# Performance work log

Measured on AMD Instinct MI355X. Metric: run time of the kernel, lower is better.

Reference implementation:

```python
import jax, jax.numpy as jnp
import numpy as np

HEAD = 8  # number of attention heads (init kwarg)


def setup_inputs() -> dict:
    key = jax.random.key(0)
    k1, k2, k3 = jax.random.split(key, 3)
    b, H, W, c = 8, 32, 32, 512
    dim = 512
    x = jax.random.normal(k1, (b, H, W, c), dtype=jnp.float32)
    # 1x1 Conv == per-pixel matmul over channels
    w_qkv = jax.random.normal(k2, (c, 3 * dim), dtype=jnp.float32) * (c ** -0.5)
    w_out = jax.random.normal(k3, (dim, dim), dtype=jnp.float32) * (dim ** -0.5)
    b_out = jnp.zeros((dim,), dtype=jnp.float32)
    return {"x": x, "w_qkv": w_qkv, "w_out": w_out, "b_out": b_out}


def reference(x, w_qkv, w_out, b_out):
    b, H, W, c = x.shape
    n = H * W
    # QKV 1x1-conv projection (no bias)
    qkv = jnp.einsum('bhwc,cd->bhwd', x, w_qkv)          # (b, H, W, 3*dim)
    qkv = qkv.reshape(b, n, HEAD, -1)                     # (b, n, head, 3*dh)
    q, k, v = jnp.split(qkv, 3, axis=-1)                  # each (b, n, head, dh)
    scale = b ** -0.5  # NOTE: source scales by batch size, reproduced faithfully
    attn = jax.nn.softmax(jnp.einsum('bihd,bjhd->bhij', q, k) * scale, axis=-1)
    out = jnp.einsum('bhij,bjhd->bihd', attn, v)          # (b, n, head, dh)
    out = out.reshape(b, H, W, -1)                        # (b, H, W, dim)
    # output 1x1-conv projection (with bias)
    return jnp.einsum('bhwc,cd->bhwd', out, w_out) + b_out
```

## Files before the change

### kernel.cpp

```cpp
#include <hip/hip_runtime.h>
#include <hip/hip_bf16.h>

typedef __bf16 bf16x8_t __attribute__((ext_vector_type(8)));
typedef float  f32x4_t  __attribute__((ext_vector_type(4)));
typedef short  s16x4_t  __attribute__((ext_vector_type(4)));
typedef short  s16x8_t  __attribute__((ext_vector_type(8)));

#define NTOK   1024
#define CDIM   512
#define QKVDIM 1536
#define NHEAD  8
#define DHEAD  64
#define C1EXP  0.51007088f
#define C2EXP  34.624681f

__device__ __forceinline__ float b2f(short s) {
    unsigned int u = ((unsigned int)(unsigned short)s) << 16;
    float f; __builtin_memcpy(&f, &u, 4); return f;
}
__device__ __forceinline__ short f2b(float f) {
    __bf16 h = (__bf16)f; short s; __builtin_memcpy(&s, &h, 2); return s;
}

__global__ __launch_bounds__(256) void cvt_w(
    const float* __restrict__ wq, const float* __restrict__ wo,
    short* __restrict__ wqbT, short* __restrict__ wobT)
{
    const int b = blockIdx.x;
    const int t = threadIdx.x;
    const int kk = t & 63, grp = t >> 6;
    if (b < 192) {
        const int K0 = (b & 7) * 64, N0 = (b >> 3) * 64;
#pragma unroll
        for (int s = 0; s < 16; ++s) {
            int n = N0 + grp * 16 + s;
            wqbT[(size_t)n * 512 + K0 + kk] = f2b(wq[(size_t)(K0 + kk) * 1536 + n]);
        }
    } else {
        const int b2 = b - 192;
        const int K0 = (b2 & 7) * 64, N0 = (b2 >> 3) * 64;
#pragma unroll
        for (int s = 0; s < 16; ++s) {
            int n = N0 + grp * 16 + s;
            wobT[(size_t)n * 512 + K0 + kk] = f2b(wo[(size_t)(K0 + kk) * 512 + n]);
        }
    }
}

__global__ __launch_bounds__(256) void gemm_qkv(
    const float* __restrict__ X, const short* __restrict__ Bt,
    short* __restrict__ qk, short* __restrict__ vT)
{
    __shared__ __align__(16) short Al[128 * 64];
    __shared__ __align__(16) short Bl[128 * 64];

    const int t = threadIdx.x;
    const int bid = blockIdx.x;
    const int xcd = bid & 7, jpos = bid >> 3;
    const int tm = xcd * 8 + jpos / 12;
    const int tn = jpos % 12;
    const int N0 = tn * 128, M0 = tm * 128;
    const int w = t >> 6, lane = t & 63;
    const int quad = lane >> 4, mr = lane & 15;
    const int wm = (w >> 1) * 64, wn = (w & 1) * 64;

    int srow[4], soff[4];
#pragma unroll
    for (int r = 0; r < 4; ++r) {
        int ci = r * 256 + t;
        srow[r] = ci >> 3;
        soff[r] = (ci & 7) * 8;
    }
    const float* Ag = X  + (size_t)M0 * 512;
    const short* Bg = Bt + (size_t)N0 * 512;

    float4  fa[4][2];
    s16x8_t br[4];
#pragma unroll
    for (int r = 0; r < 4; ++r) {
        const float* pa = Ag + (size_t)srow[r] * 512 + soff[r];
        fa[r][0] = *(const float4*)pa;
        fa[r][1] = *(const float4*)(pa + 4);
        br[r] = *(const s16x8_t*)(Bg + (size_t)srow[r] * 512 + soff[r]);
    }

    f32x4_t acc[4][4];
#pragma unroll
    for (int ms = 0; ms < 4; ++ms)
#pragma unroll
        for (int ns = 0; ns < 4; ++ns) acc[ms][ns] = f32x4_t{0.f,0.f,0.f,0.f};

#pragma unroll 1
    for (int kc = 0; kc < 8; ++kc) {
        __syncthreads();
#pragma unroll
        for (int r = 0; r < 4; ++r) {
            int lds = srow[r] * 64 + (((soff[r] >> 3) ^ (srow[r] & 7)) * 8);
            s16x8_t va;
            va[0] = f2b(fa[r][0].x); va[1] = f2b(fa[r][0].y);
            va[2] = f2b(fa[r][0].z); va[3] = f2b(fa[r][0].w);
            va[4] = f2b(fa[r][1].x); va[5] = f2b(fa[r][1].y);
            va[6] = f2b(fa[r][1].z); va[7] = f2b(fa[r][1].w);
            *(s16x8_t*)(Al + lds) = va;
            *(s16x8_t*)(Bl + lds) = br[r];
        }
        __syncthreads();
        if (kc < 7) {
            int k0 = (kc + 1) * 64;
#pragma unroll
            for (int r = 0; r < 4; ++r) {
                const float* pa = Ag + (size_t)srow[r] * 512 + k0 + soff[r];
                fa[r][0] = *(const float4*)pa;
                fa[r][1] = *(const float4*)(pa + 4);
                br[r] = *(const s16x8_t*)(Bg + (size_t)srow[r] * 512 + k0 + soff[r]);
            }
        }
#pragma unroll
        for (int kh = 0; kh < 2; ++kh) {
            bf16x8_t af[4], bf[4];
#pragma unroll
            for (int ms = 0; ms < 4; ++ms) {
                int rr = wm + ms * 16 + mr;
                af[ms] = *(const bf16x8_t*)(Al + rr * 64 + (((kh * 4 + quad) ^ (rr & 7)) * 8));
            }
#pragma unroll
            for (int ns = 0; ns < 4; ++ns) {
                int rr = wn + ns * 16 + mr;
                bf[ns] = *(const bf16x8_t*)(Bl + rr * 64 + (((kh * 4 + quad) ^ (rr & 7)) * 8));
            }
#pragma unroll
            for (int ms = 0; ms < 4; ++ms)
#pragma unroll
                for (int ns = 0; ns < 4; ++ns)
                    acc[ms][ns] = __builtin_amdgcn_mfma_f32_16x16x32_bf16(
                        af[ms], bf[ns], acc[ms][ns], 0, 0, 0);
        }
    }

#pragma unroll
    for (int ms = 0; ms < 4; ++ms) {
        int row = M0 + wm + ms * 16 + quad * 4;
        int bb = row >> 10, ti = row & 1023;
#pragma unroll
        for (int ns = 0; ns < 4; ++ns) {
            int c0 = N0 + wn + ns * 16;
            int hh = c0 / 192, r0 = c0 % 192;
            if (r0 < 128) {
                size_t base = (size_t)row * 1024 + hh * 128 + r0 + mr;
#pragma unroll
                for (int i = 0; i < 4; ++i)
                    qk[base + (size_t)i * 1024] = f2b(acc[ms][ns][i]);
            } else {
                s16x4_t v4;
#pragma unroll
                for (int i = 0; i < 4; ++i) v4[i] = f2b(acc[ms][ns][i]);
                *(s16x4_t*)(vT + ((size_t)(bb * 8 + hh) * 64 + (r0 - 128) + mr) * 1024 + ti) = v4;
            }
        }
    }
}

template <int N, bool BIAS, bool OUTF32>
__global__ __launch_bounds__(256) void gemm128(
    const short* __restrict__ A, const short* __restrict__ Bt,
    const float* __restrict__ bias, void* __restrict__ C)
{
    __shared__ __align__(16) short Al[128 * 64];
    __shared__ __align__(16) short Bl[128 * 64];

    constexpr int TNT = N / 128;
    const int t = threadIdx.x;
    const int bid = blockIdx.x;
    const int xcd = bid & 7, jpos = bid >> 3;
    const int tm = xcd * 8 + jpos / TNT;
    const int tn = jpos % TNT;
    const int N0 = tn * 128, M0 = tm * 128;
    const int w = t >> 6, lane = t & 63;
    const int quad = lane >> 4, mr = lane & 15;
    const int wm = (w >> 1) * 64, wn = (w & 1) * 64;

    int srow[4], soff[4];
#pragma unroll
    for (int r = 0; r < 4; ++r) {
        int ci = r * 256 + t;
        srow[r] = ci >> 3;
        soff[r] = (ci & 7) * 8;
    }
    const short* Ag = A  + (size_t)M0 * 512;
    const short* Bg = Bt + (size_t)N0 * 512;

    s16x8_t ar[4], br[4];
#pragma unroll
    for (int r = 0; r < 4; ++r) {
        ar[r] = *(const s16x8_t*)(Ag + (size_t)srow[r] * 512 + soff[r]);
        br[r] = *(const s16x8_t*)(Bg + (size_t)srow[r] * 512 + soff[r]);
    }

    f32x4_t acc[4][4];
#pragma unroll
    for (int ms = 0; ms < 4; ++ms)
#pragma unroll
        for (int ns = 0; ns < 4; ++ns) acc[ms][ns] = f32x4_t{0.f,0.f,0.f,0.f};

#pragma unroll 1
    for (int kc = 0; kc < 8; ++kc) {
        __syncthreads();
#pragma unroll
        for (int r = 0; r < 4; ++r) {
            int lds = srow[r] * 64 + (((soff[r] >> 3) ^ (srow[r] & 7)) * 8);
            *(s16x8_t*)(Al + lds) = ar[r];
            *(s16x8_t*)(Bl + lds) = br[r];
        }
        __syncthreads();
        if (kc < 7) {
            int k0 = (kc + 1) * 64;
#pragma unroll
            for (int r = 0; r < 4; ++r) {
                ar[r] = *(const s16x8_t*)(Ag + (size_t)srow[r] * 512 + k0 + soff[r]);
                br[r] = *(const s16x8_t*)(Bg + (size_t)srow[r] * 512 + k0 + soff[r]);
            }
        }
#pragma unroll
        for (int kh = 0; kh < 2; ++kh) {
            bf16x8_t af[4], bf[4];
#pragma unroll
            for (int ms = 0; ms < 4; ++ms) {
                int rr = wm + ms * 16 + mr;
                af[ms] = *(const bf16x8_t*)(Al + rr * 64 + (((kh * 4 + quad) ^ (rr & 7)) * 8));
            }
#pragma unroll
            for (int ns = 0; ns < 4; ++ns) {
                int rr = wn + ns * 16 + mr;
                bf[ns] = *(const bf16x8_t*)(Bl + rr * 64 + (((kh * 4 + quad) ^ (rr & 7)) * 8));
            }
#pragma unroll
            for (int ms = 0; ms < 4; ++ms)
#pragma unroll
                for (int ns = 0; ns < 4; ++ns)
                    acc[ms][ns] = __builtin_amdgcn_mfma_f32_16x16x32_bf16(
                        af[ms], bf[ns], acc[ms][ns], 0, 0, 0);
        }
    }

#pragma unroll
    for (int ms = 0; ms < 4; ++ms) {
        int row = M0 + wm + ms * 16 + quad * 4;
#pragma unroll
        for (int ns = 0; ns < 4; ++ns) {
            int col = N0 + wn + ns * 16 + mr;
            float bz = BIAS ? bias[col] : 0.f;
#pragma unroll
            for (int i = 0; i < 4; ++i) {
                if constexpr (OUTF32)
                    ((float*)C)[(size_t)(row + i) * N + col] = acc[ms][ns][i] + bz;
                else
                    ((short*)C)[(size_t)(row + i) * N + col] = f2b(acc[ms][ns][i]);
            }
        }
    }
}

__global__ __launch_bounds__(256) void attn_st(
    const short* __restrict__ qk, const short* __restrict__ vT,
    short* __restrict__ aout)
{
    __shared__ __align__(16) short Kl[64 * 72];
    __shared__ __align__(16) short Vt[64 * 72];
    __shared__ __align__(16) short Pl[4][16 * 72];

    const int t = threadIdx.x;
    const int g = blockIdx.x;
    const int qt = (g >> 3) & 15;
    const int bh = ((g >> 7) << 3) | (g & 7);
    const int h = bh & 7, b = bh >> 3;
    const int w = t >> 6, lane = t & 63;
    const int quad = lane >> 4, mr = lane & 15;

    const size_t qbase = (size_t)(b * NTOK + qt * 64 + w * 16 + mr) * 1024 + h * 128;
    const bf16x8_t qf0 = *(const bf16x8_t*)(qk + qbase + quad * 8);
    const bf16x8_t qf1 = *(const bf16x8_t*)(qk + qbase + 32 + quad * 8);

    s16x8_t ones_s;
#pragma unroll
    for (int e = 0; e < 8; ++e) ones_s[e] = 0x3F80;
    const bf16x8_t onesv = *(const bf16x8_t*)&ones_s;

    f32x4_t L4 = f32x4_t{0.f, 0.f, 0.f, 0.f};
    f32x4_t O[4];
#pragma unroll
    for (int d = 0; d < 4; ++d) O[d] = f32x4_t{0.f, 0.f, 0.f, 0.f};

    short* Pm = Pl[w];

    const int r0i = t >> 3, r1i = r0i + 32, c8 = (t & 7) * 8;
    const size_t kgbase = (size_t)(b * NTOK) * 1024 + h * 128 + 64 + c8;
    const size_t vgbase = (size_t)(b * 8 + h) * 64 * 1024 + c8;

    s16x8_t k0r, k1r, v0r, v1r;
    k0r = *(const s16x8_t*)(qk + kgbase + (size_t)r0i * 1024);
    k1r = *(const s16x8_t*)(qk + kgbase + (size_t)r1i * 1024);
    v0r = *(const s16x8_t*)(vT + vgbase + (size_t)r0i * 1024);
    v1r = *(const s16x8_t*)(vT + vgbase + (size_t)r1i * 1024);

#pragma unroll 1
    for (int jt = 0; jt < 16; ++jt) {
        *(s16x8_t*)(Kl + r0i * 72 + c8) = k0r;
        *(s16x8_t*)(Kl + r1i * 72 + c8) = k1r;
        *(s16x8_t*)(Vt + r0i * 72 + c8) = v0r;
        *(s16x8_t*)(Vt + r1i * 72 + c8) = v1r;
        __syncthreads();

        if (jt < 15) {
            int j0n = (jt + 1) * 64;
            k0r = *(const s16x8_t*)(qk + kgbase + (size_t)(j0n + r0i) * 1024);
            k1r = *(const s16x8_t*)(qk + kgbase + (size_t)(j0n + r1i) * 1024);
            v0r = *(const s16x8_t*)(vT + vgbase + (size_t)r0i * 1024 + j0n);
            v1r = *(const s16x8_t*)(vT + vgbase + (size_t)r1i * 1024 + j0n);
        }

        f32x4_t s[4];
        __builtin_amdgcn_s_setprio(1);
#pragma unroll
        for (int jj = 0; jj < 4; ++jj) {
            const short* kb = Kl + (jj * 16 + mr) * 72 + quad * 8;
            f32x4_t a0 = __builtin_amdgcn_mfma_f32_16x16x32_bf16(
                *(const bf16x8_t*)kb, qf0, f32x4_t{0.f,0.f,0.f,0.f}, 0, 0, 0);
            s[jj] = __builtin_amdgcn_mfma_f32_16x16x32_bf16(
                *(const bf16x8_t*)(kb + 32), qf1, a0, 0, 0, 0);
        }
        __builtin_amdgcn_s_setprio(0);

#pragma unroll
        for (int jj = 0; jj < 4; ++jj) {
            s16x4_t pv;
#pragma unroll
            for (int r = 0; r < 4; ++r)
                pv[r] = f2b(__builtin_amdgcn_exp2f(s[jj][r] * C1EXP - C2EXP));
            *(s16x4_t*)(Pm + mr * 72 + jj * 16 + quad * 4) = pv;
        }

        bf16x8_t pa0 = *(const bf16x8_t*)(Pm + mr * 72 + quad * 8);
        bf16x8_t pa1 = *(const bf16x8_t*)(Pm + mr * 72 + 32 + quad * 8);

        __builtin_amdgcn_s_setprio(1);
        L4 = __builtin_amdgcn_mfma_f32_16x16x32_bf16(pa0, onesv, L4, 0, 0, 0);
        L4 = __builtin_amdgcn_mfma_f32_16x16x32_bf16(pa1, onesv, L4, 0, 0, 0);
#pragma unroll
        for (int dt = 0; dt < 4; ++dt) {
            const short* vb = Vt + (dt * 16 + mr) * 72 + quad * 8;
            O[dt] = __builtin_amdgcn_mfma_f32_16x16x32_bf16(
                pa0, *(const bf16x8_t*)vb, O[dt], 0, 0, 0);
            O[dt] = __builtin_amdgcn_mfma_f32_16x16x32_bf16(
                pa1, *(const bf16x8_t*)(vb + 32), O[dt], 0, 0, 0);
        }
        __builtin_amdgcn_s_setprio(0);
        __syncthreads();
    }

#pragma unroll
    for (int dt = 0; dt < 4; ++dt)
#pragma unroll
        for (int i = 0; i < 4; ++i)
            Pm[(quad * 4 + i) * 72 + dt * 16 + mr] = f2b(O[dt][i] * (1.f / L4[i]));
    __syncthreads();

    const int q2 = lane >> 2, h2 = lane & 3;
    const size_t tok = (size_t)(b * NTOK + qt * 64 + w * 16 + q2);
    s16x8_t o0 = *(const s16x8_t*)(Pm + q2 * 72 + h2 * 16);
    s16x8_t o1 = *(const s16x8_t*)(Pm + q2 * 72 + h2 * 16 + 8);
    *(s16x8_t*)(aout + tok * CDIM + h * DHEAD + h2 * 16)     = o0;
    *(s16x8_t*)(aout + tok * CDIM + h * DHEAD + h2 * 16 + 8) = o1;
}

extern "C" void kernel_launch(void* const* d_in, const int* in_sizes, int n_in,
                              void* d_out, int out_size, void* d_ws, size_t ws_size,
                              hipStream_t stream)
{
    const float* x     = (const float*)d_in[0];
    const float* w_qkv = (const float*)d_in[1];
    const float* w_out = (const float*)d_in[2];
    const float* b_out = (const float*)d_in[3];
    for (int i = 0; i < n_in; ++i) {
        if      (in_sizes[i] == 4194304) x     = (const float*)d_in[i];
        else if (in_sizes[i] ==  786432) w_qkv = (const float*)d_in[i];
        else if (in_sizes[i] ==  262144) w_out = (const float*)d_in[i];
        else if (in_sizes[i] ==     512) b_out = (const float*)d_in[i];
    }

    short* qk   = (short*)d_ws;
    short* vT   = (short*)((char*)d_ws + (size_t)8192 * 1024 * 2);
    short* aout = (short*)((char*)d_ws + (size_t)8192 * 1024 * 2 + (size_t)64 * 64 * 1024 * 2);
    short* wobT = (short*)((char*)d_ws + (size_t)33 * 1024 * 1024 + (size_t)1664 * 1024);
    short* wqbT = (short*)d_out + (size_t)8192 * 512;

    cvt_w<<<256, 256, 0, stream>>>(w_qkv, w_out, wqbT, wobT);

    gemm_qkv<<<768, 256, 0, stream>>>(x, wqbT, qk, vT);

    attn_st<<<1024, 256, 0, stream>>>(qk, vT, aout);

    gemm128<CDIM, true, true>
        <<<(CDIM / 128) * 64, 256, 0, stream>>>(aout, wobT, b_out, d_out);
}
```

Baseline: 135.7 us.

## Enlarge attention tiles to 128 queries and 128 keys per block

The attention kernel now runs 512-thread blocks (8 waves) that each handle 128 query rows and stage 128-key K/V tiles per iteration, which halves the grid and the number of loop iterations and barriers. Each K/V tile loaded into shared memory is reused by twice as many query rows, cutting global K/V traffic per query. The QK^T, exp and P writeback are interleaved per 16-key sub-tile. In exchange, shared memory per block and register pressure rise, and there are fewer blocks to spread across CUs, which can reduce occupancy and latency hiding.

```diff
diff --git a/kernel.cpp b/kernel.cpp
--- a/kernel.cpp
+++ b/kernel.cpp
@@ -260,23 +260,23 @@
     }
 }
 
-__global__ __launch_bounds__(256) void attn_st(
+__global__ __launch_bounds__(512, 4) void attn_st(
     const short* __restrict__ qk, const short* __restrict__ vT,
     short* __restrict__ aout)
 {
-    __shared__ __align__(16) short Kl[64 * 72];
-    __shared__ __align__(16) short Vt[64 * 72];
-    __shared__ __align__(16) short Pl[4][16 * 72];
+    __shared__ __align__(16) short Kl[128 * 72];
+    __shared__ __align__(16) short Vt[64 * 136];
+    __shared__ __align__(16) short Pl[8][16 * 136];
 
     const int t = threadIdx.x;
     const int g = blockIdx.x;
-    const int qt = (g >> 3) & 15;
-    const int bh = ((g >> 7) << 3) | (g & 7);
+    const int qt = (g >> 3) & 7;
+    const int bh = ((g >> 6) << 3) | (g & 7);
     const int h = bh & 7, b = bh >> 3;
     const int w = t >> 6, lane = t & 63;
     const int quad = lane >> 4, mr = lane & 15;
 
-    const size_t qbase = (size_t)(b * NTOK + qt * 64 + w * 16 + mr) * 1024 + h * 128;
+    const size_t qbase = (size_t)(b * NTOK + qt * 128 + w * 16 + mr) * 1024 + h * 128;
     const bf16x8_t qf0 = *(const bf16x8_t*)(qk + qbase + quad * 8);
     const bf16x8_t qf1 = *(const bf16x8_t*)(qk + qbase + 32 + quad * 8);
 
@@ -292,68 +292,70 @@
 
     short* Pm = Pl[w];
 
-    const int r0i = t >> 3, r1i = r0i + 32, c8 = (t & 7) * 8;
-    const size_t kgbase = (size_t)(b * NTOK) * 1024 + h * 128 + 64 + c8;
-    const size_t vgbase = (size_t)(b * 8 + h) * 64 * 1024 + c8;
+    const int kr0 = t >> 3, kr1 = kr0 + 64;
+    const int kc8 = (t & 7) * 8;
+    const int vr0 = t >> 4, vr1 = vr0 + 32;
+    const int vc8 = (t & 15) * 8;
+
+    const size_t kg = (size_t)(b * NTOK) * 1024 + h * 128 + 64 + kc8;
+    const size_t vg = (size_t)(b * 8 + h) * 64 * 1024 + vc8;
 
     s16x8_t k0r, k1r, v0r, v1r;
-    k0r = *(const s16x8_t*)(qk + kgbase + (size_t)r0i * 1024);
-    k1r = *(const s16x8_t*)(qk + kgbase + (size_t)r1i * 1024);
-    v0r = *(const s16x8_t*)(vT + vgbase + (size_t)r0i * 1024);
-    v1r = *(const s16x8_t*)(vT + vgbase + (size_t)r1i * 1024);
+    k0r = *(const s16x8_t*)(qk + kg + (size_t)kr0 * 1024);
+    k1r = *(const s16x8_t*)(qk + kg + (size_t)kr1 * 1024);
+    v0r = *(const s16x8_t*)(vT + vg + (size_t)vr0 * 1024);
+    v1r = *(const s16x8_t*)(vT + vg + (size_t)vr1 * 1024);
 
 #pragma unroll 1
-    for (int jt = 0; jt < 16; ++jt) {
-        *(s16x8_t*)(Kl + r0i * 72 + c8) = k0r;
-        *(s16x8_t*)(Kl + r1i * 72 + c8) = k1r;
-        *(s16x8_t*)(Vt + r0i * 72 + c8) = v0r;
-        *(s16x8_t*)(Vt + r1i * 72 + c8) = v1r;
-        __syncthreads();
-
-        if (jt < 15) {
-            int j0n = (jt + 1) * 64;
-            k0r = *(const s16x8_t*)(qk + kgbase + (size_t)(j0n + r0i) * 1024);
-            k1r = *(const s16x8_t*)(qk + kgbase + (size_t)(j0n + r1i) * 1024);
-            v0r = *(const s16x8_t*)(vT + vgbase + (size_t)r0i * 1024 + j0n);
-            v1r = *(const s16x8_t*)(vT + vgbase + (size_t)r1i * 1024 + j0n);
-        }
-
-        f32x4_t s[4];
-        __builtin_amdgcn_s_setprio(1);
-#pragma unroll
-        for (int jj = 0; jj < 4; ++jj) {
+    for (int jt = 0; jt < 8; ++jt) {
+        *(s16x8_t*)(Kl + kr0 * 72 + kc8)  = k0r;
+        *(s16x8_t*)(Kl + kr1 * 72 + kc8)  = k1r;
+        *(s16x8_t*)(Vt + vr0 * 136 + vc8) = v0r;
+        *(s16x8_t*)(Vt + vr1 * 136 + vc8) = v1r;
+        __syncthreads();
+
+        if (jt < 7) {
+            int j0n = (jt + 1) * 128;
+            k0r = *(const s16x8_t*)(qk + kg + (size_t)(j0n + kr0) * 1024);
+            k1r = *(const s16x8_t*)(qk + kg + (size_t)(j0n + kr1) * 1024);
+            v0r = *(const s16x8_t*)(vT + vg + (size_t)vr0 * 1024 + j0n);
+            v1r = *(const s16x8_t*)(vT + vg + (size_t)vr1 * 1024 + j0n);
+        }
+
+#pragma unroll
+        for (int jj = 0; jj < 8; ++jj) {
             const short* kb = Kl + (jj * 16 + mr) * 72 + quad * 8;
+            __builtin_amdgcn_s_setprio(1);
             f32x4_t a0 = __builtin_amdgcn_mfma_f32_16x16x32_bf16(
                 *(const bf16x8_t*)kb, qf0, f32x4_t{0.f,0.f,0.f,0.f}, 0, 0, 0);
-            s[jj] = __builtin_amdgcn_mfma_f32_16x16x32_bf16(
+            f32x4_t s = __builtin_amdgcn_mfma_f32_16x16x32_bf16(
                 *(const bf16x8_t*)(kb + 32), qf1, a0, 0, 0, 0);
+            __builtin_amdgcn_s_setprio(0);
+            s16x4_t pv;
+#pragma unroll
+            for (int r = 0; r < 4; ++r)
+                pv[r] = f2b(__builtin_amdgcn_exp2f(s[r] * C1EXP - C2EXP));
+            *(s16x4_t*)(Pm + mr * 136 + jj * 16 + quad * 4) = pv;
+        }
+
+        bf16x8_t pa[4];
+#pragma unroll
+        for (int ks = 0; ks < 4; ++ks)
+            pa[ks] = *(const bf16x8_t*)(Pm + mr * 136 + ks * 32 + quad * 8);
+
+        __builtin_amdgcn_s_setprio(1);
+#pragma unroll
+        for (int ks = 0; ks < 4; ++ks)
+            L4 = __builtin_amdgcn_mfma_f32_16x16x32_bf16(pa[ks], onesv, L4, 0, 0, 0);
+#pragma unroll
+        for (int dt = 0; dt < 4; ++dt) {
+            const short* vb = Vt + (dt * 16 + mr) * 136 + quad * 8;
+#pragma unroll
+            for (int ks = 0; ks < 4; ++ks)
+                O[dt] = __builtin_amdgcn_mfma_f32_16x16x32_bf16(
+                    pa[ks], *(const bf16x8_t*)(vb + ks * 32), O[dt], 0, 0, 0);
         }
         __builtin_amdgcn_s_setprio(0);
-
-#pragma unroll
-        for (int jj = 0; jj < 4; ++jj) {
-            s16x4_t pv;
-#pragma unroll
-            for (int r = 0; r < 4; ++r)
-                pv[r] = f2b(__builtin_amdgcn_exp2f(s[jj][r] * C1EXP - C2EXP));
-            *(s16x4_t*)(Pm + mr * 72 + jj * 16 + quad * 4) = pv;
-        }
-
-        bf16x8_t pa0 = *(const bf16x8_t*)(Pm + mr * 72 + quad * 8);
-        bf16x8_t pa1 = *(const bf16x8_t*)(Pm + mr * 72 + 32 + quad * 8);
-
-        __builtin_amdgcn_s_setprio(1);
-        L4 = __builtin_amdgcn_mfma_f32_16x16x32_bf16(pa0, onesv, L4, 0, 0, 0);
-        L4 = __builtin_amdgcn_mfma_f32_16x16x32_bf16(pa1, onesv, L4, 0, 0, 0);
-#pragma unroll
-        for (int dt = 0; dt < 4; ++dt) {
-            const short* vb = Vt + (dt * 16 + mr) * 72 + quad * 8;
-            O[dt] = __builtin_amdgcn_mfma_f32_16x16x32_bf16(
-                pa0, *(const bf16x8_t*)vb, O[dt], 0, 0, 0);
-            O[dt] = __builtin_amdgcn_mfma_f32_16x16x32_bf16(
-                pa1, *(const bf16x8_t*)(vb + 32), O[dt], 0, 0, 0);
-        }
-        __builtin_amdgcn_s_setprio(0);
         __syncthreads();
     }
 
@@ -361,13 +363,13 @@
     for (int dt = 0; dt < 4; ++dt)
 #pragma unroll
         for (int i = 0; i < 4; ++i)
-            Pm[(quad * 4 + i) * 72 + dt * 16 + mr] = f2b(O[dt][i] * (1.f / L4[i]));
+            Pm[(quad * 4 + i) * 136 + dt * 16 + mr] = f2b(O[dt][i] * (1.f / L4[i]));
     __syncthreads();
 
     const int q2 = lane >> 2, h2 = lane & 3;
-    const size_t tok = (size_t)(b * NTOK + qt * 64 + w * 16 + q2);
-    s16x8_t o0 = *(const s16x8_t*)(Pm + q2 * 72 + h2 * 16);
-    s16x8_t o1 = *(const s16x8_t*)(Pm + q2 * 72 + h2 * 16 + 8);
+    const size_t tok = (size_t)(b * NTOK + qt * 128 + w * 16 + q2);
+    s16x8_t o0 = *(const s16x8_t*)(Pm + q2 * 136 + h2 * 16);
+    s16x8_t o1 = *(const s16x8_t*)(Pm + q2 * 136 + h2 * 16 + 8);
     *(s16x8_t*)(aout + tok * CDIM + h * DHEAD + h2 * 16)     = o0;
     *(s16x8_t*)(aout + tok * CDIM + h * DHEAD + h2 * 16 + 8) = o1;
 }
@@ -397,7 +399,7 @@
 
     gemm_qkv<<<768, 256, 0, stream>>>(x, wqbT, qk, vT);
 
-    attn_st<<<1024, 256, 0, stream>>>(qk, vT, aout);
+    attn_st<<<512, 512, 0, stream>>>(qk, vT, aout);
 
     gemm128<CDIM, true, true>
         <<<(CDIM / 128) * 64, 256, 0, stream>>>(aout, wobT, b_out, d_out);
```

New measurement: 135.3 us. Within noise of the previous version (-0.3%).
